# Kernel optimization log

Hardware: AMD Instinct MI355X
Metric: run time of the kernel (lower is better)

The kernel has to match this reference:

```python
import jax, jax.numpy as jnp
import numpy as np

QN = 127.0  # 2^(8-1)-1, symmetric int8
EPS = 1e-5  # batchnorm eps

def ste_round(v):
    return v + jax.lax.stop_gradient(jnp.round(v) - v)

def quant_act(x):
    # HAWQ-style symmetric per-tensor activation quantization (8-bit)
    s = jnp.maximum(jnp.max(jnp.abs(x)) / QN, 1e-8)
    xq = jnp.clip(ste_round(x / s), -QN - 1.0, QN)
    return xq * s, s

def setup_inputs() -> dict:
    key = jax.random.key(0)
    k1, k2, k3, k4, k5, k6 = jax.random.split(key, 6)
    B, Cin, Cout, H, W = 128, 768, 192, 17, 17
    x = jax.random.normal(k1, (B, Cin, H, W), dtype=jnp.float32)
    conv_w = jax.random.normal(k2, (Cout, Cin, 1, 1), dtype=jnp.float32) * 0.02
    bn_gamma = 1.0 + 0.1 * jax.random.normal(k3, (Cout,), dtype=jnp.float32)
    bn_beta = 0.1 * jax.random.normal(k4, (Cout,), dtype=jnp.float32)
    bn_mean = 0.1 * jax.random.normal(k5, (Cout,), dtype=jnp.float32)
    bn_var = 0.5 + jax.random.uniform(k6, (Cout,), dtype=jnp.float32)
    return {"x": x, "conv_w": conv_w, "bn_gamma": bn_gamma, "bn_beta": bn_beta,
            "bn_mean": bn_mean, "bn_var": bn_var, "cluster": 0}

def reference(x, conv_w, bn_gamma, bn_beta, bn_mean, bn_var, cluster):
    # 1) QuantAct on raw input
    x1, s0 = quant_act(x)
    # 2) QuantAveragePool2d (k=3, s=1, p=1, count_include_pad=True): pool in integer domain
    x_int = ste_round(x1 / s0)
    pooled_sum = jax.lax.reduce_window(x_int, 0.0, jax.lax.add,
                                       (1, 1, 3, 3), (1, 1, 1, 1),
                                       [(0, 0), (0, 0), (1, 1), (1, 1)])
    x2 = (pooled_sum / 9.0) * s0
    # 3) QuantAct after pool
    x3, s1 = quant_act(x2)
    # 4) QuantBnConv2d: fold BN into 1x1 conv, per-channel symmetric weight quant
    std = jnp.sqrt(bn_var + EPS)
    w_fold = conv_w * (bn_gamma / std)[:, None, None, None]          # [O,C,1,1]
    b_fold = bn_beta - bn_gamma * bn_mean / std                      # [O]
    w_sf = jnp.maximum(jnp.max(jnp.abs(w_fold), axis=(1, 2, 3)) / QN, 1e-8)  # [O]
    w_int = jnp.clip(ste_round(w_fold / w_sf[:, None, None, None]), -QN - 1.0, QN)
    xi = x3 / s1                                                     # integer-valued acts
    b_int = ste_round(b_fold / (w_sf * s1))
    out_int = jnp.einsum('bchw,oc->bohw', xi, w_int[:, :, 0, 0]) + b_int[None, :, None, None]
    out = out_int * (w_sf * s1)[None, :, None, None]
    # 5) ReLU + output QuantAct
    out = jax.nn.relu(out)
    outq, s2 = quant_act(out)
    return outq, s2
```

## Files before the change

### kernel.cpp

```cpp
#include <hip/hip_runtime.h>
#include <math.h>

#define B_    128
#define C_    768
#define O_    192
#define HW_   289
#define N_IN  (128*768*289)
#define N_OUT (128*192*289)
#define QN_   127.0f

#define SLAB_E   (32*289)
#define SLAB_SH  9248
#define SLAB_BYT 18496
#define QP_LDS   (32*380)

typedef __attribute__((ext_vector_type(8))) short bf16x8;
typedef __attribute__((ext_vector_type(4))) float f32x4;

#define SWZ(b) ((b) ^ ((((b) >> 6) & 3) << 4))


__global__ void k_absmax_x(const float4* __restrict__ x4, int n4, unsigned* cnt) {
    float m = 0.f;
    const int stride = gridDim.x * blockDim.x;
    int i = blockIdx.x * blockDim.x + threadIdx.x;
    for (; i + stride < n4; i += 2 * stride) {
        float4 v = x4[i];
        float4 w = x4[i + stride];
        m = fmaxf(m, fmaxf(fmaxf(fabsf(v.x), fabsf(v.y)),
                           fmaxf(fabsf(v.z), fabsf(v.w))));
        m = fmaxf(m, fmaxf(fmaxf(fabsf(w.x), fabsf(w.y)),
                           fmaxf(fabsf(w.z), fabsf(w.w))));
    }
    if (i < n4) {
        float4 v = x4[i];
        m = fmaxf(m, fmaxf(fmaxf(fabsf(v.x), fabsf(v.y)),
                           fmaxf(fabsf(v.z), fabsf(v.w))));
    }
#pragma unroll
    for (int off = 32; off; off >>= 1) m = fmaxf(m, __shfl_down(m, off));
    __shared__ float sm[4];
    int lane = threadIdx.x & 63, wv = threadIdx.x >> 6;
    if (lane == 0) sm[wv] = m;
    __syncthreads();
    if (threadIdx.x == 0) {
        float bm = fmaxf(fmaxf(sm[0], sm[1]), fmaxf(sm[2], sm[3]));
        atomicMax(cnt + 0, __float_as_uint(bm));
    }
}

__launch_bounds__(512) __global__
void k_quant_pool(const float* __restrict__ x, short* __restrict__ pooled,
                  unsigned* cnt) {
    __shared__ __align__(16) float fq[QP_LDS + 8];
    __shared__ int smax[8];
    const int tid = threadIdx.x;
    const int kt = blockIdx.x;
    const int b = blockIdx.z;
    const float s0 = fmaxf(__uint_as_float(cnt[0]) / QN_, 1e-8f);

    for (int i = tid; i < QP_LDS + 8; i += 512) fq[i] = 0.f;
    __syncthreads();

    const float4* xg4 = (const float4*)(x + ((size_t)b * 768 + kt * 32) * HW_);
    for (int t = tid; t < SLAB_E / 4; t += 512) {
        float4 v = xg4[t];
        float q0 = rintf(v.x / s0);
        float q1 = rintf(v.y / s0);
        float q2 = rintf(v.z / s0);
        float q3 = rintf(v.w / s0);
        int e = 4 * t;
#pragma unroll
        for (int j = 0; j < 4; ++j) {
            float q = (j == 0) ? q0 : (j == 1) ? q1 : (j == 2) ? q2 : q3;
            int ej = e + j;
            int p = (ej * 29027) >> 23;
            int i2 = ej - p * 289;
            int r = (i2 * 3856) >> 16;
            int c = i2 - r * 17;
            fq[p * 380 + (r + 1) * 20 + (c + 1)] = q;
        }
    }
    __syncthreads();

    short* slab = pooled + (size_t)(b * 24 + kt) * SLAB_SH;
    int tmax = 0;
    for (int task = tid; task < 2720; task += 512) {
        int p = task & 31;
        int rt = task >> 5;
        int r = (rt * 3277) >> 14;
        int t5 = rt - r * 5;
        int c0 = t5 * 4;
        const float* base = fq + p * 380 + r * 20 + c0;
        float4 a0 = *(const float4*)(base);
        float4 a1 = *(const float4*)(base + 4);
        float4 b0 = *(const float4*)(base + 20);
        float4 b1 = *(const float4*)(base + 24);
        float4 d0 = *(const float4*)(base + 40);
        float4 d1 = *(const float4*)(base + 44);
        float s0c = a0.x + b0.x + d0.x;
        float s1c = a0.y + b0.y + d0.y;
        float s2c = a0.z + b0.z + d0.z;
        float s3c = a0.w + b0.w + d0.w;
        float s4c = a1.x + b1.x + d1.x;
        float s5c = a1.y + b1.y + d1.y;
        int o0 = (int)(s0c + s1c + s2c);
        int o1 = (int)(s1c + s2c + s3c);
        int o2 = (int)(s2c + s3c + s4c);
        int o3 = (int)(s3c + s4c + s5c);
        int i0 = r * 17 + c0;
        slab[(i0 + 0) * 32 + p] = (short)o0;
        int a = o0 < 0 ? -o0 : o0; tmax = a > tmax ? a : tmax;
        if (c0 + 1 < 17) {
            slab[(i0 + 1) * 32 + p] = (short)o1;
            a = o1 < 0 ? -o1 : o1; tmax = a > tmax ? a : tmax;
            slab[(i0 + 2) * 32 + p] = (short)o2;
            a = o2 < 0 ? -o2 : o2; tmax = a > tmax ? a : tmax;
            slab[(i0 + 3) * 32 + p] = (short)o3;
            a = o3 < 0 ? -o3 : o3; tmax = a > tmax ? a : tmax;
        }
    }

#pragma unroll
    for (int off = 32; off; off >>= 1) {
        int o = __shfl_down(tmax, off);
        tmax = o > tmax ? o : tmax;
    }
    if ((tid & 63) == 0) smax[tid >> 6] = tmax;
    __syncthreads();
    if (tid == 0) {
        int bm = smax[0];
#pragma unroll
        for (int i = 1; i < 8; ++i) bm = smax[i] > bm ? smax[i] : bm;
        atomicMax((int*)(cnt + 1), bm);
    }
}

__global__ void k_weights(const float* __restrict__ conv_w,
                          const float* __restrict__ g,
                          const float* __restrict__ beta,
                          const float* __restrict__ mu,
                          const float* __restrict__ var,
                          const unsigned* __restrict__ cnt,
                          unsigned short* __restrict__ w_q,
                          float* __restrict__ b_int, float* __restrict__ scale_o,
                          unsigned short* __restrict__ lut) {
    if (blockIdx.x == O_) {
        const float s0 = fmaxf(__uint_as_float(cnt[0]) / QN_, 1e-8f);
        const float maxx2 = ((float)((const int*)cnt)[1] / 9.0f) * s0;
        const float s1 = fmaxf(maxx2 / QN_, 1e-8f);
        for (int i = threadIdx.x; i < 2305; i += 256) {
            float p = (float)(i - 1152);
            float t = (p / 9.0f) * s0;
            float v = rintf(t / s1);
            v = fminf(fmaxf(v, -128.f), 127.f);
            lut[i] = (unsigned short)(__float_as_uint(v) >> 16);
        }
        return;
    }
    const int o = blockIdx.x;
    const float stdv = sqrtf(var[o] + 1e-5f);
    const float r = g[o] / stdv;
    const float* wo = conv_w + o * C_;
    float m = 0.f;
    for (int c = threadIdx.x; c < C_; c += 256) m = fmaxf(m, fabsf(wo[c] * r));
#pragma unroll
    for (int off = 32; off; off >>= 1) m = fmaxf(m, __shfl_down(m, off));
    __shared__ float sm[4];
    __shared__ float swsf;
    int lane = threadIdx.x & 63, wv = threadIdx.x >> 6;
    if (lane == 0) sm[wv] = m;
    __syncthreads();
    if (threadIdx.x == 0) {
        float bm = fmaxf(fmaxf(sm[0], sm[1]), fmaxf(sm[2], sm[3]));
        swsf = fmaxf(bm / QN_, 1e-8f);
    }
    __syncthreads();
    const float wsf = swsf;
    for (int c = threadIdx.x; c < C_; c += 256) {
        float wi = rintf(wo[c] * r / wsf);
        wi = fminf(fmaxf(wi, -128.f), 127.f);
        w_q[(c >> 5) * 6144 + o * 32 + (c & 31)] =
            (unsigned short)(__float_as_uint(wi) >> 16);
    }
    if (threadIdx.x == 0) {
        float s0 = fmaxf(__uint_as_float(cnt[0]) / QN_, 1e-8f);
        float maxx2 = ((float)((const int*)cnt)[1] / 9.0f) * s0;
        float s1 = fmaxf(maxx2 / QN_, 1e-8f);
        float bf = beta[o] - g[o] * mu[o] / stdv;
        b_int[o] = rintf(bf / (wsf * s1));
        scale_o[o] = wsf * s1;
    }
}

__launch_bounds__(256) __global__
void k_gemm(const short* __restrict__ pooled,
            const unsigned short* __restrict__ w_q,
            const unsigned short* __restrict__ lut_g,
            const float* __restrict__ b_int, const float* __restrict__ scale_o,
            unsigned* cnt, float* __restrict__ out) {
    __shared__ char sW[2][12288];
    __shared__ char sX[2][5120];
    __shared__ unsigned short s_lut[2305];
    __shared__ float red[4];
    const int tid = threadIdx.x;
    const int b = blockIdx.z;
    const int hw0 = blockIdx.x * 80;
    const int L = tid & 63;
    const int wv = tid >> 6;
    const int wo = wv * 48;
    const char* pooled_b = (const char*)pooled;

    for (int i = tid; i < 2305; i += 256) s_lut[i] = lut_g[i];

    const int hwr0 = tid >> 2, cg0 = tid & 3;
    const int hwr1 = 64 + (tid >> 2), cg1 = tid & 3;
    const bool act1 = tid < 64;
    const int hwg0 = hw0 + hwr0, hwg1 = hw0 + hwr1;

    uint4 xr0, xr1;

    auto stageW = [&](int kt, int buf) {
#pragma unroll
        for (int j = 0; j < 3; ++j) {
            int ldsoff = (wv * 3 + j) * 1024;
            const char* src = (const char*)w_q + kt * 12288 + SWZ(ldsoff + L * 16);
            __builtin_amdgcn_global_load_lds(
                (const __attribute__((address_space(1))) unsigned int*)src,
                (__attribute__((address_space(3))) unsigned int*)(&sW[buf][0] + ldsoff),
                16, 0, 0);
        }
    };
    auto loadX = [&](int kt) {
        uint4 z; z.x = z.y = z.z = z.w = 0u;
        size_t slab = (size_t)(b * 24 + kt) * SLAB_BYT;
        xr0 = (hwg0 < HW_)
            ? *(const uint4*)(pooled_b + slab + hwg0 * 64 + cg0 * 16) : z;
        if (act1)
            xr1 = (hwg1 < HW_)
                ? *(const uint4*)(pooled_b + slab + hwg1 * 64 + cg1 * 16) : z;
    };
    auto writeX = [&](int buf) {
        uint4 q;
        q.x = (unsigned)s_lut[1152 + (short)(xr0.x)] |
              ((unsigned)s_lut[1152 + (short)(xr0.x >> 16)] << 16);
        q.y = (unsigned)s_lut[1152 + (short)(xr0.y)] |
              ((unsigned)s_lut[1152 + (short)(xr0.y >> 16)] << 16);
        q.z = (unsigned)s_lut[1152 + (short)(xr0.z)] |
              ((unsigned)s_lut[1152 + (short)(xr0.z >> 16)] << 16);
        q.w = (unsigned)s_lut[1152 + (short)(xr0.w)] |
              ((unsigned)s_lut[1152 + (short)(xr0.w >> 16)] << 16);
        *(uint4*)(&sX[buf][0] + SWZ(hwr0 * 64 + cg0 * 16)) = q;
        if (act1) {
            uint4 p2;
            p2.x = (unsigned)s_lut[1152 + (short)(xr1.x)] |
                   ((unsigned)s_lut[1152 + (short)(xr1.x >> 16)] << 16);
            p2.y = (unsigned)s_lut[1152 + (short)(xr1.y)] |
                   ((unsigned)s_lut[1152 + (short)(xr1.y >> 16)] << 16);
            p2.z = (unsigned)s_lut[1152 + (short)(xr1.z)] |
                   ((unsigned)s_lut[1152 + (short)(xr1.z >> 16)] << 16);
            p2.w = (unsigned)s_lut[1152 + (short)(xr1.w)] |
                   ((unsigned)s_lut[1152 + (short)(xr1.w >> 16)] << 16);
            *(uint4*)(&sX[buf][0] + SWZ(hwr1 * 64 + cg1 * 16)) = p2;
        }
    };

    f32x4 acc[3][5] = {};

    stageW(0, 0);
    loadX(0);
    __syncthreads();
    writeX(0);
    __syncthreads();

    for (int kt = 0; kt < 24; ++kt) {
        const int cur = kt & 1, nxt = cur ^ 1;
        if (kt < 23) {
            stageW(kt + 1, nxt);
            loadX(kt + 1);
        }
        bf16x8 af[3], bfr[5];
#pragma unroll
        for (int m = 0; m < 3; ++m)
            af[m] = *(const bf16x8*)(&sW[cur][0] +
                SWZ((wo + m * 16 + (L & 15)) * 64 + (L >> 4) * 16));
#pragma unroll
        for (int n = 0; n < 5; ++n)
            bfr[n] = *(const bf16x8*)(&sX[cur][0] +
                SWZ((n * 16 + (L & 15)) * 64 + (L >> 4) * 16));
#pragma unroll
        for (int m = 0; m < 3; ++m)
#pragma unroll
            for (int n = 0; n < 5; ++n)
                acc[m][n] = __builtin_amdgcn_mfma_f32_16x16x32_bf16(
                    af[m], bfr[n], acc[m][n], 0, 0, 0);
        if (kt < 23) writeX(nxt);
        __syncthreads();
    }

    float lmax = 0.f;
#pragma unroll
    for (int m = 0; m < 3; ++m) {
        int ob = wo + m * 16 + (L >> 4) * 4;
        float bi0 = b_int[ob + 0], bi1 = b_int[ob + 1];
        float bi2 = b_int[ob + 2], bi3 = b_int[ob + 3];
        float sc0 = scale_o[ob + 0], sc1 = scale_o[ob + 1];
        float sc2 = scale_o[ob + 2], sc3 = scale_o[ob + 3];
#pragma unroll
        for (int n = 0; n < 5; ++n) {
            int hw = hw0 + n * 16 + (L & 15);
            if (hw < HW_) {
                size_t base = ((size_t)b * O_ + ob) * HW_ + hw;
                float v0 = fmaxf((acc[m][n][0] + bi0) * sc0, 0.f);
                float v1 = fmaxf((acc[m][n][1] + bi1) * sc1, 0.f);
                float v2 = fmaxf((acc[m][n][2] + bi2) * sc2, 0.f);
                float v3 = fmaxf((acc[m][n][3] + bi3) * sc3, 0.f);
                out[base + 0 * HW_] = v0;
                out[base + 1 * HW_] = v1;
                out[base + 2 * HW_] = v2;
                out[base + 3 * HW_] = v3;
                lmax = fmaxf(fmaxf(fmaxf(v0, v1), fmaxf(v2, v3)), lmax);
            }
        }
    }
#pragma unroll
    for (int off = 32; off; off >>= 1) lmax = fmaxf(lmax, __shfl_down(lmax, off));
    if (L == 0) red[wv] = lmax;
    __syncthreads();
    if (tid == 0) {
        float bm = fmaxf(fmaxf(red[0], red[1]), fmaxf(red[2], red[3]));
        atomicMax(cnt + 2, __float_as_uint(bm));
    }
}

__global__ void k_quant_out(float* __restrict__ out, const unsigned* __restrict__ cnt) {
    const float s2 = fmaxf(__uint_as_float(cnt[2]) / QN_, 1e-8f);
    float4* o4 = (float4*)out;
    const int n4 = N_OUT / 4;
    for (int i = blockIdx.x * blockDim.x + threadIdx.x; i < n4;
         i += gridDim.x * blockDim.x) {
        float4 v = o4[i];
        v.x = fminf(fmaxf(rintf(v.x / s2), -128.f), 127.f) * s2;
        v.y = fminf(fmaxf(rintf(v.y / s2), -128.f), 127.f) * s2;
        v.z = fminf(fmaxf(rintf(v.z / s2), -128.f), 127.f) * s2;
        v.w = fminf(fmaxf(rintf(v.w / s2), -128.f), 127.f) * s2;
        o4[i] = v;
    }
    if (blockIdx.x == 0 && threadIdx.x == 0) out[N_OUT] = s2;
}

extern "C" void kernel_launch(void* const* d_in, const int* in_sizes, int n_in,
                              void* d_out, int out_size, void* d_ws, size_t ws_size,
                              hipStream_t stream) {
    const float* x      = (const float*)d_in[0];
    const float* conv_w = (const float*)d_in[1];
    const float* g      = (const float*)d_in[2];
    const float* beta   = (const float*)d_in[3];
    const float* mu     = (const float*)d_in[4];
    const float* var    = (const float*)d_in[5];
    float* out = (float*)d_out;

    char* wsb = (char*)d_ws;
    unsigned* cnt          = (unsigned*)wsb;
    float* b_int           = (float*)(wsb + 1024);
    float* scale_o         = (float*)(wsb + 2048);
    unsigned short* lut    = (unsigned short*)(wsb + 3072);
    unsigned short* w_q    = (unsigned short*)(wsb + 8192);
    short* pooled          = (short*)(wsb + (1u << 20));

    hipMemsetAsync(cnt, 0, 16, stream);
    k_absmax_x<<<2048, 256, 0, stream>>>((const float4*)x, N_IN / 4, cnt);
    dim3 qgrid(24, 1, B_);
    k_quant_pool<<<qgrid, 512, 0, stream>>>(x, pooled, cnt);
    k_weights<<<O_ + 1, 256, 0, stream>>>(conv_w, g, beta, mu, var, cnt, w_q,
                                          b_int, scale_o, lut);
    dim3 ggrid(4, 1, B_);
    k_gemm<<<ggrid, 256, 0, stream>>>(pooled, w_q, lut, b_int, scale_o, cnt, out);
    k_quant_out<<<2048, 256, 0, stream>>>(out, cnt);
}
```

Baseline: 143.6 us.

## Switch 1x1 conv GEMM from bf16 MFMA to int8 MFMA

New measurement: 132.3 us. 7.9% less time.

```diff
diff --git a/kernel.cpp b/kernel.cpp
--- a/kernel.cpp
+++ b/kernel.cpp
@@ -14,8 +14,7 @@
 #define SLAB_BYT 18496
 #define QP_LDS   (32*380)
 
-typedef __attribute__((ext_vector_type(8))) short bf16x8;
-typedef __attribute__((ext_vector_type(4))) float f32x4;
+typedef __attribute__((ext_vector_type(4))) int i32x4;
 
 #define SWZ(b) ((b) ^ ((((b) >> 6) & 3) << 4))
 
@@ -142,9 +141,9 @@
                           const float* __restrict__ mu,
                           const float* __restrict__ var,
                           const unsigned* __restrict__ cnt,
-                          unsigned short* __restrict__ w_q,
+                          signed char* __restrict__ w_q8,
                           float* __restrict__ b_int, float* __restrict__ scale_o,
-                          unsigned short* __restrict__ lut) {
+                          unsigned char* __restrict__ lut8) {
     if (blockIdx.x == O_) {
         const float s0 = fmaxf(__uint_as_float(cnt[0]) / QN_, 1e-8f);
         const float maxx2 = ((float)((const int*)cnt)[1] / 9.0f) * s0;
@@ -154,7 +153,7 @@
             float t = (p / 9.0f) * s0;
             float v = rintf(t / s1);
             v = fminf(fmaxf(v, -128.f), 127.f);
-            lut[i] = (unsigned short)(__float_as_uint(v) >> 16);
+            lut8[i] = (unsigned char)(signed char)(int)v;
         }
         return;
     }
@@ -180,8 +179,7 @@
     for (int c = threadIdx.x; c < C_; c += 256) {
         float wi = rintf(wo[c] * r / wsf);
         wi = fminf(fmaxf(wi, -128.f), 127.f);
-        w_q[(c >> 5) * 6144 + o * 32 + (c & 31)] =
-            (unsigned short)(__float_as_uint(wi) >> 16);
+        w_q8[(c >> 6) * 12288 + o * 64 + (c & 63)] = (signed char)(int)wi;
     }
     if (threadIdx.x == 0) {
         float s0 = fmaxf(__uint_as_float(cnt[0]) / QN_, 1e-8f);
@@ -195,13 +193,13 @@
 
 __launch_bounds__(256) __global__
 void k_gemm(const short* __restrict__ pooled,
-            const unsigned short* __restrict__ w_q,
-            const unsigned short* __restrict__ lut_g,
+            const signed char* __restrict__ w_q8,
+            const unsigned char* __restrict__ lut8,
             const float* __restrict__ b_int, const float* __restrict__ scale_o,
             unsigned* cnt, float* __restrict__ out) {
     __shared__ char sW[2][12288];
     __shared__ char sX[2][5120];
-    __shared__ unsigned short s_lut[2305];
+    __shared__ unsigned char s_lut[2305];
     __shared__ float red[4];
     const int tid = threadIdx.x;
     const int b = blockIdx.z;
@@ -211,61 +209,59 @@
     const int wo = wv * 48;
     const char* pooled_b = (const char*)pooled;
 
-    for (int i = tid; i < 2305; i += 256) s_lut[i] = lut_g[i];
-
-    const int hwr0 = tid >> 2, cg0 = tid & 3;
-    const int hwr1 = 64 + (tid >> 2), cg1 = tid & 3;
-    const bool act1 = tid < 64;
-    const int hwg0 = hw0 + hwr0, hwg1 = hw0 + hwr1;
-
-    uint4 xr0, xr1;
+    for (int i = tid; i < 2305; i += 256) s_lut[i] = lut8[i];
+
+    const int row0 = tid >> 3, ch0 = tid & 7;
+    const int row1 = 32 + (tid >> 3), ch1 = tid & 7;
+    const int row2 = 64 + (tid >> 3), ch2 = tid & 7;
+    const bool act2 = tid < 128;
+
+    uint4 xr0, xr1, xr2;
 
     auto stageW = [&](int kt, int buf) {
 #pragma unroll
         for (int j = 0; j < 3; ++j) {
             int ldsoff = (wv * 3 + j) * 1024;
-            const char* src = (const char*)w_q + kt * 12288 + SWZ(ldsoff + L * 16);
+            const char* src = (const char*)w_q8 + kt * 12288 + SWZ(ldsoff + L * 16);
             __builtin_amdgcn_global_load_lds(
                 (const __attribute__((address_space(1))) unsigned int*)src,
                 (__attribute__((address_space(3))) unsigned int*)(&sW[buf][0] + ldsoff),
                 16, 0, 0);
         }
     };
+    auto ldx = [&](int kt, int row, int ch) -> uint4 {
+        uint4 z; z.x = z.y = z.z = z.w = 0u;
+        int hw = hw0 + row;
+        if (hw >= HW_) return z;
+        size_t slab = (size_t)(b * 24 + 2 * kt + (ch >> 2)) * SLAB_BYT;
+        return *(const uint4*)(pooled_b + slab + hw * 64 + (ch & 3) * 16);
+    };
     auto loadX = [&](int kt) {
-        uint4 z; z.x = z.y = z.z = z.w = 0u;
-        size_t slab = (size_t)(b * 24 + kt) * SLAB_BYT;
-        xr0 = (hwg0 < HW_)
-            ? *(const uint4*)(pooled_b + slab + hwg0 * 64 + cg0 * 16) : z;
-        if (act1)
-            xr1 = (hwg1 < HW_)
-                ? *(const uint4*)(pooled_b + slab + hwg1 * 64 + cg1 * 16) : z;
+        xr0 = ldx(kt, row0, ch0);
+        xr1 = ldx(kt, row1, ch1);
+        if (act2) xr2 = ldx(kt, row2, ch2);
+    };
+    auto pack8 = [&](const uint4& v) -> uint2 {
+        unsigned c0 = s_lut[1152 + (short)(v.x)];
+        unsigned c1 = s_lut[1152 + (short)(v.x >> 16)];
+        unsigned c2 = s_lut[1152 + (short)(v.y)];
+        unsigned c3 = s_lut[1152 + (short)(v.y >> 16)];
+        unsigned c4 = s_lut[1152 + (short)(v.z)];
+        unsigned c5 = s_lut[1152 + (short)(v.z >> 16)];
+        unsigned c6 = s_lut[1152 + (short)(v.w)];
+        unsigned c7 = s_lut[1152 + (short)(v.w >> 16)];
+        uint2 r;
+        r.x = c0 | (c1 << 8) | (c2 << 16) | (c3 << 24);
+        r.y = c4 | (c5 << 8) | (c6 << 16) | (c7 << 24);
+        return r;
     };
     auto writeX = [&](int buf) {
-        uint4 q;
-        q.x = (unsigned)s_lut[1152 + (short)(xr0.x)] |
-              ((unsigned)s_lut[1152 + (short)(xr0.x >> 16)] << 16);
-        q.y = (unsigned)s_lut[1152 + (short)(xr0.y)] |
-              ((unsigned)s_lut[1152 + (short)(xr0.y >> 16)] << 16);
-        q.z = (unsigned)s_lut[1152 + (short)(xr0.z)] |
-              ((unsigned)s_lut[1152 + (short)(xr0.z >> 16)] << 16);
-        q.w = (unsigned)s_lut[1152 + (short)(xr0.w)] |
-              ((unsigned)s_lut[1152 + (short)(xr0.w >> 16)] << 16);
-        *(uint4*)(&sX[buf][0] + SWZ(hwr0 * 64 + cg0 * 16)) = q;
-        if (act1) {
-            uint4 p2;
-            p2.x = (unsigned)s_lut[1152 + (short)(xr1.x)] |
-                   ((unsigned)s_lut[1152 + (short)(xr1.x >> 16)] << 16);
-            p2.y = (unsigned)s_lut[1152 + (short)(xr1.y)] |
-                   ((unsigned)s_lut[1152 + (short)(xr1.y >> 16)] << 16);
-            p2.z = (unsigned)s_lut[1152 + (short)(xr1.z)] |
-                   ((unsigned)s_lut[1152 + (short)(xr1.z >> 16)] << 16);
-            p2.w = (unsigned)s_lut[1152 + (short)(xr1.w)] |
-                   ((unsigned)s_lut[1152 + (short)(xr1.w >> 16)] << 16);
-            *(uint4*)(&sX[buf][0] + SWZ(hwr1 * 64 + cg1 * 16)) = p2;
-        }
-    };
-
-    f32x4 acc[3][5] = {};
+        *(uint2*)(&sX[buf][0] + SWZ(row0 * 64 + ch0 * 8)) = pack8(xr0);
+        *(uint2*)(&sX[buf][0] + SWZ(row1 * 64 + ch1 * 8)) = pack8(xr1);
+        if (act2) *(uint2*)(&sX[buf][0] + SWZ(row2 * 64 + ch2 * 8)) = pack8(xr2);
+    };
+
+    i32x4 acc[3][5] = {};
 
     stageW(0, 0);
     loadX(0);
@@ -273,28 +269,28 @@
     writeX(0);
     __syncthreads();
 
-    for (int kt = 0; kt < 24; ++kt) {
+    for (int kt = 0; kt < 12; ++kt) {
         const int cur = kt & 1, nxt = cur ^ 1;
-        if (kt < 23) {
+        if (kt < 11) {
             stageW(kt + 1, nxt);
             loadX(kt + 1);
         }
-        bf16x8 af[3], bfr[5];
+        i32x4 af[3], bfr[5];
 #pragma unroll
         for (int m = 0; m < 3; ++m)
-            af[m] = *(const bf16x8*)(&sW[cur][0] +
+            af[m] = *(const i32x4*)(&sW[cur][0] +
                 SWZ((wo + m * 16 + (L & 15)) * 64 + (L >> 4) * 16));
 #pragma unroll
         for (int n = 0; n < 5; ++n)
-            bfr[n] = *(const bf16x8*)(&sX[cur][0] +
+            bfr[n] = *(const i32x4*)(&sX[cur][0] +
                 SWZ((n * 16 + (L & 15)) * 64 + (L >> 4) * 16));
 #pragma unroll
         for (int m = 0; m < 3; ++m)
 #pragma unroll
             for (int n = 0; n < 5; ++n)
-                acc[m][n] = __builtin_amdgcn_mfma_f32_16x16x32_bf16(
+                acc[m][n] = __builtin_amdgcn_mfma_i32_16x16x64_i8(
                     af[m], bfr[n], acc[m][n], 0, 0, 0);
-        if (kt < 23) writeX(nxt);
+        if (kt < 11) writeX(nxt);
         __syncthreads();
     }
 
@@ -311,10 +307,10 @@
             int hw = hw0 + n * 16 + (L & 15);
             if (hw < HW_) {
                 size_t base = ((size_t)b * O_ + ob) * HW_ + hw;
-                float v0 = fmaxf((acc[m][n][0] + bi0) * sc0, 0.f);
-                float v1 = fmaxf((acc[m][n][1] + bi1) * sc1, 0.f);
-                float v2 = fmaxf((acc[m][n][2] + bi2) * sc2, 0.f);
-                float v3 = fmaxf((acc[m][n][3] + bi3) * sc3, 0.f);
+                float v0 = fmaxf(((float)acc[m][n][0] + bi0) * sc0, 0.f);
+                float v1 = fmaxf(((float)acc[m][n][1] + bi1) * sc1, 0.f);
+                float v2 = fmaxf(((float)acc[m][n][2] + bi2) * sc2, 0.f);
+                float v3 = fmaxf(((float)acc[m][n][3] + bi3) * sc3, 0.f);
                 out[base + 0 * HW_] = v0;
                 out[base + 1 * HW_] = v1;
                 out[base + 2 * HW_] = v2;
@@ -364,17 +360,17 @@
     unsigned* cnt          = (unsigned*)wsb;
     float* b_int           = (float*)(wsb + 1024);
     float* scale_o         = (float*)(wsb + 2048);
-    unsigned short* lut    = (unsigned short*)(wsb + 3072);
-    unsigned short* w_q    = (unsigned short*)(wsb + 8192);
+    unsigned char* lut8    = (unsigned char*)(wsb + 3072);
+    signed char* w_q8      = (signed char*)(wsb + 8192);
     short* pooled          = (short*)(wsb + (1u << 20));
 
     hipMemsetAsync(cnt, 0, 16, stream);
     k_absmax_x<<<2048, 256, 0, stream>>>((const float4*)x, N_IN / 4, cnt);
     dim3 qgrid(24, 1, B_);
     k_quant_pool<<<qgrid, 512, 0, stream>>>(x, pooled, cnt);
-    k_weights<<<O_ + 1, 256, 0, stream>>>(conv_w, g, beta, mu, var, cnt, w_q,
-                                          b_int, scale_o, lut);
+    k_weights<<<O_ + 1, 256, 0, stream>>>(conv_w, g, beta, mu, var, cnt, w_q8,
+                                          b_int, scale_o, lut8);
     dim3 ggrid(4, 1, B_);
-    k_gemm<<<ggrid, 256, 0, stream>>>(pooled, w_q, lut, b_int, scale_o, cnt, out);
+    k_gemm<<<ggrid, 256, 0, stream>>>(pooled, w_q8, lut8, b_int, scale_o, cnt, out);
     k_quant_out<<<2048, 256, 0, stream>>>(out, cnt);
 }
```
